# Optimization experiments

Measured on AMD Instinct MI355X. Metric: run time of the kernel, lower is better.

## Reference

```python
import jax, jax.numpy as jnp
import numpy as np

# NFFT config (matches torch NFFT(N=(256,256), m=4, sigma=2.0))
N = (256, 256)          # output Fourier grid
n = (512, 512)          # oversampled grid (2*(int(sigma*N)//2))
m = 4                   # window half-width -> (2m)^2 = 64 taps per point
B, C, M = 2, 2, 200000  # batch, channels, nonuniform points
SIGMA = tuple(n[i] / N[i] for i in range(2))  # KaiserBesselWindow sigma = n/N


def kb_phi(k):
    """Kaiser-Bessel window phi(k), k: (..., 2). Matches KaiserBesselWindow.forward."""
    nv = jnp.asarray(n, dtype=k.dtype)
    b = (2.0 - 1.0 / jnp.asarray(SIGMA, dtype=k.dtype)) * jnp.pi
    t = m * m - (nv * k) ** 2
    safe = t > 0
    arg = jnp.sqrt(jnp.where(safe, t, 1.0))
    out = jnp.where(safe, jnp.sinh(b * arg) / (arg * jnp.pi), 0.0)  # nan_to_num(...,0) equiv.
    return jnp.prod(out, axis=-1)


def kb_phi_hat():
    """Fourier coefficients of the window on the N-grid (KaiserBesselWindow.ft)."""
    grids = jnp.meshgrid(*[jnp.arange(-(N[i] // 2), N[i] // 2, dtype=jnp.float32)
                           for i in range(2)], indexing='ij')
    inds = jnp.stack(grids, axis=-1)                                 # (N1,N2,2)
    nv = jnp.asarray(n, jnp.float32)
    b = (2.0 - 1.0 / jnp.asarray(SIGMA, jnp.float32)) * jnp.pi
    ft = jnp.i0(m * jnp.sqrt(b ** 2 - (2.0 * jnp.pi * inds / nv) ** 2))
    return jnp.prod(ft, axis=-1)                                     # (N1,N2)


def setup_inputs() -> dict:
    key = jax.random.key(0)
    k1, k2, k3 = jax.random.split(key, 3)
    x = jax.random.uniform(k1, (B, 1, M, 2), dtype=jnp.float32) - 0.5  # points in [-1/2,1/2)
    f_hat_real = jax.random.normal(k2, (B, C, N[0], N[1]), dtype=jnp.float32)
    f_hat_imag = jax.random.normal(k3, (B, C, N[0], N[1]), dtype=jnp.float32)
    return {"x": x, "f_hat_real": f_hat_real, "f_hat_imag": f_hat_imag}


def reference(x, f_hat_real, f_hat_imag):
    f_hat = f_hat_real + 1j * f_hat_imag                              # (B,C,N1,N2) complex64
    # deconvolve by window Fourier coefficients
    g_hat = f_hat / kb_phi_hat()
    # zero-pad to oversampled grid n
    cut = [(n[i] - N[i]) // 2 for i in range(2)]
    g_hat = jnp.pad(g_hat, ((0, 0), (0, 0), (cut[0], cut[0]), (cut[1], cut[1])))
    ax = (-2, -1)
    g = jnp.fft.ifftshift(jnp.fft.fft2(jnp.fft.fftshift(g_hat, ax), norm='backward'), ax)
    # windowed gather (sparse_convolution): (2m)^2 taps per nonuniform point
    r = jnp.arange(2 * m, dtype=jnp.int32)
    off = jnp.stack(jnp.meshgrid(r, r, indexing='ij'), axis=-1).reshape(-1, 2)  # (64,2)
    nv = jnp.asarray(n, jnp.float32)
    base = jnp.ceil(x * nv).astype(jnp.int32) - m                     # (B,1,M,2)
    inds = base[None] + off[:, None, None, None, :]                   # (64,B,1,M,2)
    w = kb_phi(x[None] - inds.astype(jnp.float32) / nv)               # (64,B,1,M)
    half = jnp.asarray([n[0] // 2, n[1] // 2], jnp.int32)
    nn = jnp.asarray(n, jnp.int32)
    im = (inds + half) % nn                                           # wrap onto grid
    g2 = jnp.transpose(g, (0, 2, 3, 1))                               # (B,n1,n2,C)
    bidx = jnp.arange(B, dtype=jnp.int32)[None, :, None, None]
    gl = g2[bidx, im[..., 0], im[..., 1]]                             # (64,B,1,M,C)
    f = jnp.sum(gl * w[..., None].astype(gl.dtype), axis=0)           # (B,1,M,C)
    return jnp.transpose(f[:, 0], (0, 2, 1))                          # (B,C,M) complex64
```

## Files before the change

### kernel.cpp

```cpp
#include <hip/hip_runtime.h>
#include <math.h>


#define NGRID 512
#define NSMALL 256
#define MW 4
#define BB 2
#define CC 2
#define MPTS 200000
#define PLANE (BB * CC * MPTS)
#define LPAD4 513
#define IMG4 (NGRID * NGRID)
#define G16OFF(b) ((size_t)(b) * 524288 + 131072)

__device__ __forceinline__ float nfft29781_i0_large(float z) {
    float inv = 1.0f / z;
    float p = 1.0f + inv * (0.125f + inv * (0.0703125f
              + inv * (0.0732421875f + inv * 0.112152099609375f)));
    return expf(z) * rsqrtf(2.0f * (float)M_PI * z) * p;
}

__device__ __forceinline__ int nfft29781_brev9(int v) {
    return (int)(__brev((unsigned)v) >> 23);
}

__device__ __forceinline__ unsigned nfft29781_bf16pack(float a, float b) {
    unsigned ua = __float_as_uint(a);
    ua += 0x7FFFu + ((ua >> 16) & 1u);
    unsigned ub = __float_as_uint(b);
    ub += 0x7FFFu + ((ub >> 16) & 1u);
    return (ua >> 16) | (ub & 0xFFFF0000u);
}

__device__ __forceinline__ void nfft29781_fft512_c2(float4* s, int tid) {
    #pragma unroll
    for (int st = 0; st < 9; ++st) {
        int half = 1 << st;
        int pos = tid & (half - 1);
        int i0 = ((tid >> st) << (st + 1)) + pos;
        int i1 = i0 + half;
        float ang = -(float)M_PI * (float)pos / (float)half;
        float sn, cs;
        __sincosf(ang, &sn, &cs);
        float4 a = s[i0];
        float4 b = s[i1];
        float4 tw;
        tw.x = b.x * cs - b.y * sn;  tw.y = b.x * sn + b.y * cs;
        tw.z = b.z * cs - b.w * sn;  tw.w = b.z * sn + b.w * cs;
        s[i0] = make_float4(a.x + tw.x, a.y + tw.y, a.z + tw.z, a.w + tw.w);
        s[i1] = make_float4(a.x - tw.x, a.y - tw.y, a.z - tw.z, a.w - tw.w);
        __syncthreads();
    }
}

__global__ __launch_bounds__(256) void nfft29781_rows2(const float* __restrict__ fr,
                                                       const float* __restrict__ fi,
                                                       float4* __restrict__ G32) {
    __shared__ float4 s[NGRID];
    int tid = threadIdx.x;
    int b   = blockIdx.x >> 8;
    int a1  = blockIdx.x & 255;

    const float bcon  = 1.5f * (float)M_PI;
    const float scale = 2.0f * (float)M_PI / (float)NGRID;
    float k1 = (float)(a1 - 128) * scale;
    float p1 = nfft29781_i0_large((float)MW * sqrtf(bcon * bcon - k1 * k1));

    int a2 = tid ^ 128;
    float k2 = (float)(a2 - 128) * scale;
    float p2 = nfft29781_i0_large((float)MW * sqrtf(bcon * bcon - k2 * k2));
    float invp = 1.0f / (p1 * p2);

    size_t s0 = ((size_t)(b * CC + 0) * NSMALL + a1) * NSMALL + a2;
    size_t s1 = ((size_t)(b * CC + 1) * NSMALL + a1) * NSMALL + a2;
    float4 v = make_float4(fr[s0] * invp, fi[s0] * invp,
                           fr[s1] * invp, fi[s1] * invp);

    int j2v = (tid < 128) ? tid : tid + 256;
    int j2z = (tid < 128) ? tid + 256 : tid;
    s[nfft29781_brev9(j2v)] = v;
    s[nfft29781_brev9(j2z)] = make_float4(0.0f, 0.0f, 0.0f, 0.0f);
    __syncthreads();

    nfft29781_fft512_c2(s, tid);

    int j1 = (a1 < 128) ? a1 + 384 : a1 - 128;
    float4* Gb = G32 + (size_t)b * IMG4 + (size_t)j1 * NGRID;
    Gb[tid]       = s[tid];
    Gb[tid + 256] = s[tid + 256];
}

__global__ __launch_bounds__(256) void nfft29781_cols2(float4* __restrict__ G32) {
    __shared__ float4 s[4 * LPAD4];
    int tid  = threadIdx.x;
    int b    = blockIdx.x >> 7;
    int col0 = (blockIdx.x & 127) << 2;
    const float4* Gb = G32 + (size_t)b * IMG4;

    #pragma unroll
    for (int it = 0; it < 4; ++it) {
        int e  = it * 256 + tid;
        int cp = e & 3;
        int q  = e >> 2;
        int r  = (q < 128) ? q : q + 256;
        s[cp * LPAD4 + nfft29781_brev9(r)] = Gb[(size_t)r * NGRID + col0 + cp];
    }
    #pragma unroll
    for (int it = 0; it < 4; ++it) {
        int e  = it * 256 + tid;
        int cp = e & 3;
        int q  = e >> 2;
        s[cp * LPAD4 + nfft29781_brev9(q + 128)] = make_float4(0.0f, 0.0f, 0.0f, 0.0f);
    }
    __syncthreads();

    int c = tid & 3;
    int w = tid >> 2;
    float4* sc = s + c * LPAD4;
    for (int st = 0; st < 9; ++st) {
        int half = 1 << st;
        #pragma unroll
        for (int k = 0; k < 4; ++k) {
            int bf  = w + (k << 6);
            int pos = bf & (half - 1);
            int i0  = ((bf >> st) << (st + 1)) + pos;
            int i1  = i0 + half;
            float ang = -(float)M_PI * (float)pos / (float)half;
            float sn, cs;
            __sincosf(ang, &sn, &cs);
            float4 a = sc[i0];
            float4 bb = sc[i1];
            float4 tw;
            tw.x = bb.x * cs - bb.y * sn;  tw.y = bb.x * sn + bb.y * cs;
            tw.z = bb.z * cs - bb.w * sn;  tw.w = bb.z * sn + bb.w * cs;
            sc[i0] = make_float4(a.x + tw.x, a.y + tw.y, a.z + tw.z, a.w + tw.w);
            sc[i1] = make_float4(a.x - tw.x, a.y - tw.y, a.z - tw.z, a.w - tw.w);
        }
        __syncthreads();
    }

    uint2* G16 = (uint2*)G32 + G16OFF(b);
    #pragma unroll
    for (int it = 0; it < 8; ++it) {
        int e  = it * 256 + tid;
        int cp = e & 3;
        int r  = e >> 2;
        float4 v = s[cp * LPAD4 + r];
        uint2 pk;
        pk.x = nfft29781_bf16pack(v.x, v.y);
        pk.y = nfft29781_bf16pack(v.z, v.w);
        G16[(size_t)r * NGRID + col0 + cp] = pk;
    }
}

__global__ __launch_bounds__(256) void nfft29781_gather_bf16(const float* __restrict__ x,
                                                             const uint2* __restrict__ G16base,
                                                             float* __restrict__ out,
                                                             int out_elems) {
    int t  = blockIdx.x * blockDim.x + threadIdx.x;
    int j  = t & 7;
    int pp = t >> 3;
    if (pp >= BB * MPTS) return;
    int b  = (pp >= MPTS) ? 1 : 0;
    int pt = pp - b * MPTS;

    float u0 = x[(size_t)pp * 2 + 0] * (float)NGRID;
    float u1 = x[(size_t)pp * 2 + 1] * (float)NGRID;

    float c0 = ceilf(u0), c1 = ceilf(u1);
    int base0 = (int)c0 - MW;
    int base1 = (int)c1 - MW;
    float d0 = c0 - u0, d1 = c1 - u1;

    const float bw = 1.5f * (float)M_PI;
    const float invpi = 1.0f / (float)M_PI;
    float w0m, w1m;
    {
        float nk = (float)(MW - j) - d0;
        float tt = (float)(MW * MW) - nk * nk;
        w0m = 0.0f;
        if (tt > 0.0f) { float a = sqrtf(tt); float e = expf(bw * a);
                         w0m = (e - 1.0f / e) * 0.5f * invpi / a; }
        nk = (float)(MW - j) - d1;
        tt = (float)(MW * MW) - nk * nk;
        w1m = 0.0f;
        if (tt > 0.0f) { float a = sqrtf(tt); float e = expf(bw * a);
                         w1m = (e - 1.0f / e) * 0.5f * invpi / a; }
    }

    const uint2* Gi = G16base + G16OFF(b);
    int cix = (base1 + j) & (NGRID - 1);
    int lanebase = (threadIdx.x & 63) & ~7;

    float a0x = 0.0f, a0y = 0.0f, a1x = 0.0f, a1y = 0.0f;
    #pragma unroll
    for (int i = 0; i < 8; ++i) {
        float w0i = __shfl(w0m, lanebase + i, 64);
        uint2 g = Gi[(size_t)(((base0 + i) & (NGRID - 1)) << 9) + cix];
        float g0x = __uint_as_float(g.x << 16);
        float g0y = __uint_as_float(g.x & 0xFFFF0000u);
        float g1x = __uint_as_float(g.y << 16);
        float g1y = __uint_as_float(g.y & 0xFFFF0000u);
        a0x += w0i * g0x;  a0y += w0i * g0y;
        a1x += w0i * g1x;  a1y += w0i * g1y;
    }
    a0x *= w1m;  a0y *= w1m;  a1x *= w1m;  a1y *= w1m;

    #pragma unroll
    for (int msk = 1; msk < 8; msk <<= 1) {
        a0x += __shfl_xor(a0x, msk, 64);
        a0y += __shfl_xor(a0y, msk, 64);
        a1x += __shfl_xor(a1x, msk, 64);
        a1y += __shfl_xor(a1y, msk, 64);
    }

    if (j == 0) {
        size_t o0 = (size_t)(b * CC) * MPTS + pt;
        size_t o1 = o0 + MPTS;
        if (o0 < (size_t)out_elems)         out[o0]         = a0x;
        if (PLANE + o0 < (size_t)out_elems) out[PLANE + o0] = a0y;
        if (o1 < (size_t)out_elems)         out[o1]         = a1x;
        if (PLANE + o1 < (size_t)out_elems) out[PLANE + o1] = a1y;
    }
}

extern "C" void kernel_launch(void* const* d_in, const int* in_sizes, int n_in,
                              void* d_out, int out_size, void* d_ws, size_t ws_size,
                              hipStream_t stream) {
    (void)in_sizes; (void)n_in;
    const float* x  = (const float*)d_in[0];
    const float* fr = (const float*)d_in[1];
    const float* fi = (const float*)d_in[2];
    float*  out = (float*)d_out;
    float4* G32 = (float4*)d_ws;

    const size_t fullBytes = (size_t)BB * IMG4 * sizeof(float4);
    if (ws_size < fullBytes) return;

    nfft29781_rows2<<<BB * NSMALL, 256, 0, stream>>>(fr, fi, G32);
    nfft29781_cols2<<<BB * (NGRID / 4), 256, 0, stream>>>(G32);
    int gthreads = BB * MPTS * 8;
    nfft29781_gather_bf16<<<(gthreads + 255) / 256, 256, 0, stream>>>(
        x, (const uint2*)d_ws, out, out_size);
}
```

Before: 99.19 us.

## Store row-FFT intermediate as compact bf16 and gather two points per thread

The row-FFT kernel now writes only the 256 nonzero rows, packed as bf16, into a compact buffer instead of a full-size float4 image. The column FFT reads those rows directly and unpacks them, which cuts intermediate memory traffic in both kernels. The gather kernel now processes two nonuniform points per 8-lane group, launching half as many threads and issuing more independent loads per thread. The cost is an extra bf16 rounding stage after the row FFT, which lowers accuracy, and more registers per gather thread.

```diff
diff --git a/kernel.cpp b/kernel.cpp
--- a/kernel.cpp
+++ b/kernel.cpp
@@ -10,8 +10,9 @@
 #define MPTS 200000
 #define PLANE (BB * CC * MPTS)
 #define LPAD4 513
-#define IMG4 (NGRID * NGRID)
-#define G16OFF(b) ((size_t)(b) * 524288 + 131072)
+#define GROWS_B 131072
+#define GCOLS_OFF 262144
+#define GCOLS_B 262144
 
 __device__ __forceinline__ float nfft29781_i0_large(float z) {
     float inv = 1.0f / z;
@@ -30,6 +31,13 @@
     unsigned ub = __float_as_uint(b);
     ub += 0x7FFFu + ((ub >> 16) & 1u);
     return (ua >> 16) | (ub & 0xFFFF0000u);
+}
+
+__device__ __forceinline__ float4 nfft29781_unpk(uint2 g) {
+    return make_float4(__uint_as_float(g.x << 16),
+                       __uint_as_float(g.x & 0xFFFF0000u),
+                       __uint_as_float(g.y << 16),
+                       __uint_as_float(g.y & 0xFFFF0000u));
 }
 
 __device__ __forceinline__ void nfft29781_fft512_c2(float4* s, int tid) {
@@ -53,9 +61,9 @@
     }
 }
 
-__global__ __launch_bounds__(256) void nfft29781_rows2(const float* __restrict__ fr,
+__global__ __launch_bounds__(256) void nfft29781_rows3(const float* __restrict__ fr,
                                                        const float* __restrict__ fi,
-                                                       float4* __restrict__ G32) {
+                                                       uint2* __restrict__ Grows) {
     __shared__ float4 s[NGRID];
     int tid = threadIdx.x;
     int b   = blockIdx.x >> 8;
@@ -84,18 +92,23 @@
 
     nfft29781_fft512_c2(s, tid);
 
-    int j1 = (a1 < 128) ? a1 + 384 : a1 - 128;
-    float4* Gb = G32 + (size_t)b * IMG4 + (size_t)j1 * NGRID;
-    Gb[tid]       = s[tid];
-    Gb[tid + 256] = s[tid + 256];
-}
-
-__global__ __launch_bounds__(256) void nfft29781_cols2(float4* __restrict__ G32) {
+    int q = a1 ^ 128;
+    uint2* Gr = Grows + ((size_t)b * NSMALL + q) * NGRID;
+    float4 v0 = s[tid], v1 = s[tid + 256];
+    uint2 pk0, pk1;
+    pk0.x = nfft29781_bf16pack(v0.x, v0.y);  pk0.y = nfft29781_bf16pack(v0.z, v0.w);
+    pk1.x = nfft29781_bf16pack(v1.x, v1.y);  pk1.y = nfft29781_bf16pack(v1.z, v1.w);
+    Gr[tid]       = pk0;
+    Gr[tid + 256] = pk1;
+}
+
+__global__ __launch_bounds__(256) void nfft29781_cols3(const uint2* __restrict__ Grows,
+                                                       uint2* __restrict__ Gcols) {
     __shared__ float4 s[4 * LPAD4];
     int tid  = threadIdx.x;
     int b    = blockIdx.x >> 7;
     int col0 = (blockIdx.x & 127) << 2;
-    const float4* Gb = G32 + (size_t)b * IMG4;
+    const uint2* Gr = Grows + (size_t)b * GROWS_B;
 
     #pragma unroll
     for (int it = 0; it < 4; ++it) {
@@ -103,7 +116,8 @@
         int cp = e & 3;
         int q  = e >> 2;
         int r  = (q < 128) ? q : q + 256;
-        s[cp * LPAD4 + nfft29781_brev9(r)] = Gb[(size_t)r * NGRID + col0 + cp];
+        s[cp * LPAD4 + nfft29781_brev9(r)] =
+            nfft29781_unpk(Gr[(size_t)q * NGRID + col0 + cp]);
     }
     #pragma unroll
     for (int it = 0; it < 4; ++it) {
@@ -139,7 +153,7 @@
         __syncthreads();
     }
 
-    uint2* G16 = (uint2*)G32 + G16OFF(b);
+    uint2* Gc = Gcols + (size_t)b * GCOLS_B;
     #pragma unroll
     for (int it = 0; it < 8; ++it) {
         int e  = it * 256 + tid;
@@ -149,78 +163,109 @@
         uint2 pk;
         pk.x = nfft29781_bf16pack(v.x, v.y);
         pk.y = nfft29781_bf16pack(v.z, v.w);
-        G16[(size_t)r * NGRID + col0 + cp] = pk;
-    }
-}
-
-__global__ __launch_bounds__(256) void nfft29781_gather_bf16(const float* __restrict__ x,
-                                                             const uint2* __restrict__ G16base,
-                                                             float* __restrict__ out,
-                                                             int out_elems) {
+        Gc[(size_t)r * NGRID + col0 + cp] = pk;
+    }
+}
+
+__global__ __launch_bounds__(256) void nfft29781_gather_x2(const float* __restrict__ x,
+                                                           const uint2* __restrict__ Gcols,
+                                                           float* __restrict__ out,
+                                                           int out_elems) {
     int t  = blockIdx.x * blockDim.x + threadIdx.x;
     int j  = t & 7;
-    int pp = t >> 3;
-    if (pp >= BB * MPTS) return;
-    int b  = (pp >= MPTS) ? 1 : 0;
-    int pt = pp - b * MPTS;
-
-    float u0 = x[(size_t)pp * 2 + 0] * (float)NGRID;
-    float u1 = x[(size_t)pp * 2 + 1] * (float)NGRID;
-
-    float c0 = ceilf(u0), c1 = ceilf(u1);
-    int base0 = (int)c0 - MW;
-    int base1 = (int)c1 - MW;
-    float d0 = c0 - u0, d1 = c1 - u1;
+    int g2 = t >> 3;
+    int pp0 = g2 * 2;
+    if (pp0 >= BB * MPTS) return;
+    int pp1 = pp0 + 1;
 
     const float bw = 1.5f * (float)M_PI;
     const float invpi = 1.0f / (float)M_PI;
-    float w0m, w1m;
+
+    int b0  = (pp0 >= MPTS) ? 1 : 0;
+    float u00 = x[(size_t)pp0 * 2 + 0] * (float)NGRID;
+    float u01 = x[(size_t)pp0 * 2 + 1] * (float)NGRID;
+    float c00 = ceilf(u00), c01 = ceilf(u01);
+    int base00 = (int)c00 - MW, base01 = (int)c01 - MW;
+    float d00 = c00 - u00, d01 = c01 - u01;
+    float w0a, w1a;
     {
-        float nk = (float)(MW - j) - d0;
+        float nk = (float)(MW - j) - d00;
         float tt = (float)(MW * MW) - nk * nk;
-        w0m = 0.0f;
-        if (tt > 0.0f) { float a = sqrtf(tt); float e = expf(bw * a);
-                         w0m = (e - 1.0f / e) * 0.5f * invpi / a; }
-        nk = (float)(MW - j) - d1;
+        w0a = 0.0f;
+        if (tt > 0.0f) { float a = sqrtf(tt); float e = expf(bw * a);
+                         w0a = (e - 1.0f / e) * 0.5f * invpi / a; }
+        nk = (float)(MW - j) - d01;
         tt = (float)(MW * MW) - nk * nk;
-        w1m = 0.0f;
-        if (tt > 0.0f) { float a = sqrtf(tt); float e = expf(bw * a);
-                         w1m = (e - 1.0f / e) * 0.5f * invpi / a; }
-    }
-
-    const uint2* Gi = G16base + G16OFF(b);
-    int cix = (base1 + j) & (NGRID - 1);
+        w1a = 0.0f;
+        if (tt > 0.0f) { float a = sqrtf(tt); float e = expf(bw * a);
+                         w1a = (e - 1.0f / e) * 0.5f * invpi / a; }
+    }
+
+    int b1  = (pp1 >= MPTS) ? 1 : 0;
+    float u10 = x[(size_t)pp1 * 2 + 0] * (float)NGRID;
+    float u11 = x[(size_t)pp1 * 2 + 1] * (float)NGRID;
+    float c10 = ceilf(u10), c11 = ceilf(u11);
+    int base10 = (int)c10 - MW, base11 = (int)c11 - MW;
+    float d10 = c10 - u10, d11 = c11 - u11;
+    float w0b, w1b;
+    {
+        float nk = (float)(MW - j) - d10;
+        float tt = (float)(MW * MW) - nk * nk;
+        w0b = 0.0f;
+        if (tt > 0.0f) { float a = sqrtf(tt); float e = expf(bw * a);
+                         w0b = (e - 1.0f / e) * 0.5f * invpi / a; }
+        nk = (float)(MW - j) - d11;
+        tt = (float)(MW * MW) - nk * nk;
+        w1b = 0.0f;
+        if (tt > 0.0f) { float a = sqrtf(tt); float e = expf(bw * a);
+                         w1b = (e - 1.0f / e) * 0.5f * invpi / a; }
+    }
+
+    const uint2* Ga = Gcols + (size_t)b0 * GCOLS_B;
+    const uint2* Gb = Gcols + (size_t)b1 * GCOLS_B;
+    int cixa = (base01 + j) & (NGRID - 1);
+    int cixb = (base11 + j) & (NGRID - 1);
     int lanebase = (threadIdx.x & 63) & ~7;
 
-    float a0x = 0.0f, a0y = 0.0f, a1x = 0.0f, a1y = 0.0f;
+    float A0 = 0.0f, A1 = 0.0f, A2 = 0.0f, A3 = 0.0f;
+    float B0 = 0.0f, B1 = 0.0f, B2 = 0.0f, B3 = 0.0f;
     #pragma unroll
     for (int i = 0; i < 8; ++i) {
-        float w0i = __shfl(w0m, lanebase + i, 64);
-        uint2 g = Gi[(size_t)(((base0 + i) & (NGRID - 1)) << 9) + cix];
-        float g0x = __uint_as_float(g.x << 16);
-        float g0y = __uint_as_float(g.x & 0xFFFF0000u);
-        float g1x = __uint_as_float(g.y << 16);
-        float g1y = __uint_as_float(g.y & 0xFFFF0000u);
-        a0x += w0i * g0x;  a0y += w0i * g0y;
-        a1x += w0i * g1x;  a1y += w0i * g1y;
-    }
-    a0x *= w1m;  a0y *= w1m;  a1x *= w1m;  a1y *= w1m;
+        float wa = __shfl(w0a, lanebase + i, 64);
+        float wb = __shfl(w0b, lanebase + i, 64);
+        uint2 ga = Ga[(size_t)((((base00 + i) & (NGRID - 1)) << 9) + cixa)];
+        uint2 gb = Gb[(size_t)((((base10 + i) & (NGRID - 1)) << 9) + cixb)];
+        float4 ua = nfft29781_unpk(ga);
+        float4 ub = nfft29781_unpk(gb);
+        A0 += wa * ua.x;  A1 += wa * ua.y;  A2 += wa * ua.z;  A3 += wa * ua.w;
+        B0 += wb * ub.x;  B1 += wb * ub.y;  B2 += wb * ub.z;  B3 += wb * ub.w;
+    }
+    A0 *= w1a;  A1 *= w1a;  A2 *= w1a;  A3 *= w1a;
+    B0 *= w1b;  B1 *= w1b;  B2 *= w1b;  B3 *= w1b;
 
     #pragma unroll
     for (int msk = 1; msk < 8; msk <<= 1) {
-        a0x += __shfl_xor(a0x, msk, 64);
-        a0y += __shfl_xor(a0y, msk, 64);
-        a1x += __shfl_xor(a1x, msk, 64);
-        a1y += __shfl_xor(a1y, msk, 64);
+        A0 += __shfl_xor(A0, msk, 64);  A1 += __shfl_xor(A1, msk, 64);
+        A2 += __shfl_xor(A2, msk, 64);  A3 += __shfl_xor(A3, msk, 64);
+        B0 += __shfl_xor(B0, msk, 64);  B1 += __shfl_xor(B1, msk, 64);
+        B2 += __shfl_xor(B2, msk, 64);  B3 += __shfl_xor(B3, msk, 64);
     }
 
     if (j == 0) {
-        size_t o0 = (size_t)(b * CC) * MPTS + pt;
-        size_t o1 = o0 + MPTS;
-        if (o0 < (size_t)out_elems)         out[o0]         = a0x;
-        if (PLANE + o0 < (size_t)out_elems) out[PLANE + o0] = a0y;
-        if (o1 < (size_t)out_elems)         out[o1]         = a1x;
-        if (PLANE + o1 < (size_t)out_elems) out[PLANE + o1] = a1y;
+        int pt0 = pp0 - b0 * MPTS;
+        int pt1 = pp1 - b1 * MPTS;
+        size_t o00 = (size_t)(b0 * CC) * MPTS + pt0;
+        size_t o01 = o00 + MPTS;
+        size_t o10 = (size_t)(b1 * CC) * MPTS + pt1;
+        size_t o11 = o10 + MPTS;
+        if (o00 < (size_t)out_elems)         out[o00]         = A0;
+        if (PLANE + o00 < (size_t)out_elems) out[PLANE + o00] = A1;
+        if (o01 < (size_t)out_elems)         out[o01]         = A2;
+        if (PLANE + o01 < (size_t)out_elems) out[PLANE + o01] = A3;
+        if (o10 < (size_t)out_elems)         out[o10]         = B0;
+        if (PLANE + o10 < (size_t)out_elems) out[PLANE + o10] = B1;
+        if (o11 < (size_t)out_elems)         out[o11]         = B2;
+        if (PLANE + o11 < (size_t)out_elems) out[PLANE + o11] = B3;
     }
 }
 
@@ -231,15 +276,15 @@
     const float* x  = (const float*)d_in[0];
     const float* fr = (const float*)d_in[1];
     const float* fi = (const float*)d_in[2];
-    float*  out = (float*)d_out;
-    float4* G32 = (float4*)d_ws;
-
-    const size_t fullBytes = (size_t)BB * IMG4 * sizeof(float4);
-    if (ws_size < fullBytes) return;
-
-    nfft29781_rows2<<<BB * NSMALL, 256, 0, stream>>>(fr, fi, G32);
-    nfft29781_cols2<<<BB * (NGRID / 4), 256, 0, stream>>>(G32);
-    int gthreads = BB * MPTS * 8;
-    nfft29781_gather_bf16<<<(gthreads + 255) / 256, 256, 0, stream>>>(
-        x, (const uint2*)d_ws, out, out_size);
-}
+    float* out  = (float*)d_out;
+    uint2* Grows = (uint2*)d_ws;
+    uint2* Gcols = (uint2*)d_ws + GCOLS_OFF;
+
+    if (ws_size < (size_t)8 * 1024 * 1024) return;
+
+    nfft29781_rows3<<<BB * NSMALL, 256, 0, stream>>>(fr, fi, Grows);
+    nfft29781_cols3<<<BB * (NGRID / 4), 256, 0, stream>>>(Grows, Gcols);
+    int gthreads = (BB * MPTS / 2) * 8;
+    nfft29781_gather_x2<<<(gthreads + 255) / 256, 256, 0, stream>>>(
+        x, Gcols, out, out_size);
+}
```

New measurement: 99.67 us. No clear change (+0.5%).
